# Kernel tuning notes

Measured on AMD Instinct MI355X. Metric: run time of the kernel, lower is better.

## Reference

```python
import jax, jax.numpy as jnp
import numpy as np

B, NSM, NLG = 64, 400, 196
SM, LG = 512, 1024
D, H, DH = 4, 16, 64
INNER = H * DH
EPS = 1e-5


def setup_inputs() -> dict:
    key = jax.random.key(0)
    ks = iter(jax.random.split(key, 40))
    def rn(shape, s=0.02):
        return jax.random.normal(next(ks), shape, jnp.float32) * s
    inp = {
        "sm_tokens": rn((B, NSM + 1, SM), 1.0),
        "lg_tokens": rn((B, NLG + 1, LG), 1.0),
    }
    def branch(p, din, dout):
        inp[p + "_pin_w"] = rn((D, din, dout))
        inp[p + "_pin_b"] = jnp.zeros((D, dout), jnp.float32)
        inp[p + "_ng"] = jnp.ones((D, dout), jnp.float32)
        inp[p + "_nb"] = jnp.zeros((D, dout), jnp.float32)
        inp[p + "_wq"] = rn((D, dout, INNER))
        inp[p + "_wkv"] = rn((D, dout, 2 * INNER))
        inp[p + "_wo"] = rn((D, INNER, dout))
        inp[p + "_wob"] = jnp.zeros((D, dout), jnp.float32)
        inp[p + "_pout_w"] = rn((D, dout, din))
        inp[p + "_pout_b"] = jnp.zeros((D, din), jnp.float32)
    branch("a", SM, LG)   # sm_attend_lg: project sm->lg, attention in lg_dim
    branch("b", LG, SM)   # lg_attend_sm: project lg->sm, attention in sm_dim
    return inp


def _attn(cls_tok, ctx, ng, nb, wq, wkv, wo, wob):
    # cls_tok: [B,1,dim]; ctx: [B,S,dim]. Matches lucidrains cross_vit Attention:
    # LayerNorm(x) first; kv context = concat(normed_x, context); context NOT normed.
    scale = DH ** -0.5
    mu = cls_tok.mean(-1, keepdims=True)
    var = ((cls_tok - mu) ** 2).mean(-1, keepdims=True)
    xn = (cls_tok - mu) * jax.lax.rsqrt(var + EPS) * ng + nb
    c = jnp.concatenate([xn, ctx], axis=1)             # kv_include_self=True
    q = (xn @ wq).reshape(B, 1, H, DH)
    k, v = jnp.split(c @ wkv, 2, axis=-1)
    k = k.reshape(B, -1, H, DH)
    v = v.reshape(B, -1, H, DH)
    s = jnp.einsum('bqhd,bkhd->bhqk', q, k) * scale     # [B,H,1,S+1]
    p = jax.nn.softmax(s, axis=-1)
    o = jnp.einsum('bhqk,bkhd->bqhd', p, v).reshape(B, 1, INNER)
    return o @ wo + wob


def _forward(sm_tokens, lg_tokens,
             a_pin_w, a_pin_b, a_ng, a_nb, a_wq, a_wkv, a_wo, a_wob, a_pout_w, a_pout_b,
             b_pin_w, b_pin_b, b_ng, b_nb, b_wq, b_wkv, b_wo, b_wob, b_pout_w, b_pout_b):
    sm_cls, sm_patch = sm_tokens[:, :1], sm_tokens[:, 1:]
    lg_cls, lg_patch = lg_tokens[:, :1], lg_tokens[:, 1:]
    for i in range(D):
        x = sm_cls @ a_pin_w[i] + a_pin_b[i]
        x = _attn(x, lg_patch, a_ng[i], a_nb[i], a_wq[i], a_wkv[i], a_wo[i], a_wob[i])
        sm_cls = x @ a_pout_w[i] + a_pout_b[i] + sm_cls
        y = lg_cls @ b_pin_w[i] + b_pin_b[i]
        y = _attn(y, sm_patch, b_ng[i], b_nb[i], b_wq[i], b_wkv[i], b_wo[i], b_wob[i])
        lg_cls = y @ b_pout_w[i] + b_pout_b[i] + lg_cls
    sm_out = jnp.concatenate([sm_cls, sm_patch], axis=1)
    lg_out = jnp.concatenate([lg_cls, lg_patch], axis=1)
    return sm_out, lg_out


def reference(sm_tokens, lg_tokens,
              a_pin_w, a_pin_b, a_ng, a_nb, a_wq, a_wkv, a_wo, a_wob, a_pout_w, a_pout_b,
              b_pin_w, b_pin_b, b_ng, b_nb, b_wq, b_wkv, b_wo, b_wob, b_pout_w, b_pout_b):
    return _forward(sm_tokens, lg_tokens,
                    a_pin_w, a_pin_b, a_ng, a_nb, a_wq, a_wkv, a_wo, a_wob, a_pout_w, a_pout_b,
                    b_pin_w, b_pin_b, b_ng, b_nb, b_wq, b_wkv, b_wo, b_wob, b_pout_w, b_pout_b)
```

## Files before the change

kernel.cpp:

```cpp
#include <hip/hip_runtime.h>
#include <hip/hip_bf16.h>
#include <math.h>

#define B_     64
#define NSM_   400
#define NLG_   196
#define SM_    512
#define LG_    1024
#define H_     16
#define DH_    64
#define INNER_ 1024
#define SSTR   424
#define PSTR   424

typedef __attribute__((ext_vector_type(8))) short bf16x8;
typedef __attribute__((ext_vector_type(8))) unsigned short u16x8;
typedef __attribute__((ext_vector_type(4))) float f32x4;

__device__ __forceinline__ unsigned short f2b(float f) {
  unsigned u = __float_as_uint(f);
  u = u + 0x7FFFu + ((u >> 16) & 1u);
  return (unsigned short)(u >> 16);
}
__device__ __forceinline__ f32x4 zero4() {
  f32x4 a; a[0] = 0.f; a[1] = 0.f; a[2] = 0.f; a[3] = 0.f; return a;
}


struct CC2 { const float* tok; float* out; unsigned short* abf; float* cls;
             unsigned short* clsb; int Np1, nf4, shift, tot4; };
struct WTDesc { const float* src; unsigned short* dst; unsigned short* dst2; int K, N; };
struct WTArgs { WTDesc d[10]; int cum[11]; };
__global__ __launch_bounds__(256) void setup1(CC2 ca, CC2 cb, WTArgs W, int nw) {
  __shared__ unsigned short tile[64][68];
  const int tid = threadIdx.x;
  if ((int)blockIdx.x < nw) {
    int bx = blockIdx.x, di = 0;
    while (bx >= W.cum[di + 1]) di++;
    int local = bx - W.cum[di];
    WTDesc g = W.d[di];
    int tn = g.N >> 6;
    int tpl = tn * (g.K >> 6);
    int layer = local / tpl, rem = local % tpl;
    int kt = (rem / tn) * 64, nt = (rem % tn) * 64;
    const float* wp = g.src + (size_t)layer * g.K * g.N;
    unsigned short* op = g.dst + (size_t)layer * g.K * g.N;
    unsigned short* d2 = (g.dst2 && nt < 1024)
                             ? g.dst2 + (size_t)layer * g.K * 1024 : nullptr;
#pragma unroll
    for (int p = 0; p < 4; p++) {
      int r = (tid >> 4) + p * 16;
      int c = (tid & 15) * 4;
      const f32x4 v = __builtin_nontemporal_load(
          (const f32x4*)&wp[(size_t)(kt + r) * g.N + nt + c]);
      ushort4 w4;
      w4.x = f2b(v.x); w4.y = f2b(v.y); w4.z = f2b(v.z); w4.w = f2b(v.w);
      *(ushort4*)&tile[r][c] = w4;
      if (d2) *(ushort4*)&d2[(size_t)(kt + r) * 1024 + nt + c] = w4;
    }
    __syncthreads();
    const int r2 = tid >> 2, cseg = tid & 3;
    u16x8 v0, v1;
#pragma unroll
    for (int i = 0; i < 8; i++) v0[i] = tile[cseg * 16 + i][r2];
#pragma unroll
    for (int i = 0; i < 8; i++) v1[i] = tile[cseg * 16 + 8 + i][r2];
    unsigned short* orow = &op[(size_t)(nt + r2) * g.K + kt + cseg * 16];
    *(u16x8*)&orow[0] = v0;
    *(u16x8*)&orow[8] = v1;
  } else {
    const int nblk = gridDim.x - nw;
    const int total = ca.tot4 + cb.tot4;
    for (int i = ((int)blockIdx.x - nw) * 256 + tid; i < total; i += nblk * 256) {
      CC2 g; int idx;
      if (i < ca.tot4) { g = ca; idx = i; } else { g = cb; idx = i - ca.tot4; }
      int rowg = idx >> g.shift, t = idx & ((1 << g.shift) - 1);
      int bb = rowg / g.Np1, row = rowg - bb * g.Np1;
      const f32x4 v = __builtin_nontemporal_load(&((const f32x4*)g.tok)[idx]);
      __builtin_nontemporal_store(v, &((f32x4*)g.out)[idx]);
      ushort4 w2; w2.x = f2b(v.x); w2.y = f2b(v.y); w2.z = f2b(v.z); w2.w = f2b(v.w);
      if (row > 0) {
        ((ushort4*)g.abf)[(size_t)(bb * (g.Np1 - 1) + row - 1) * g.nf4 + t] = w2;
      } else {
        ((f32x4*)g.cls)[(size_t)bb * g.nf4 + t] = v;
        ((ushort4*)g.clsb)[(size_t)bb * g.nf4 + t] = w2;
      }
    }
  }
}

struct TXArgs { const unsigned short* xbf; unsigned short* xT; int Nctx, dout, xstride, nx, ny, nblk; };
__global__ __launch_bounds__(256) void setup2(TXArgs ta, TXArgs tb) {
  __shared__ unsigned short tile[64][68];
  TXArgs g; int bx = blockIdx.x;
  if (bx < ta.nblk) { g = ta; } else { g = tb; bx -= ta.nblk; }
  int cx = bx % g.nx; int rem = bx / g.nx;
  int jy = rem % g.ny; int b = rem / g.ny;
  int jt = jy * 64, ct = cx * 64;
  const int tid = threadIdx.x;
#pragma unroll
  for (int p = 0; p < 4; p++) {
    int row = (tid >> 4) + p * 16;
    int c = (tid & 15) * 4;
    int j = jt + row;
    ushort4 v;
    if (j < g.Nctx) v = *(const ushort4*)&g.xbf[((size_t)b * g.Nctx + j) * g.dout + ct + c];
    else { v.x = 0; v.y = 0; v.z = 0; v.w = 0; }
    *(ushort4*)&tile[row][c] = v;
  }
  __syncthreads();
  const int r2 = tid >> 2, jseg = tid & 3;
  if (jt + jseg * 16 < g.xstride) {
    u16x8 v0, v1;
#pragma unroll
    for (int i = 0; i < 8; i++) v0[i] = tile[jseg * 16 + i][r2];
#pragma unroll
    for (int i = 0; i < 8; i++) v1[i] = tile[jseg * 16 + 8 + i][r2];
    unsigned short* orow = &g.xT[((size_t)b * g.dout + ct + r2) * g.xstride + jt + jseg * 16];
    *(u16x8*)&orow[0] = v0;
    *(u16x8*)&orow[8] = v1;
  }
}

struct SGDesc {
  const unsigned short* A; const unsigned short* WT; const float* bias;
  float* Cf; unsigned short* Cbf; const float* Rf;
  int K, N;
  float* outF; int ostride;
};
struct SGArgs { SGDesc d[4]; int cum[5]; int nd; };
__global__ __launch_bounds__(256) void sg_wide(SGArgs W) {
  int bx = blockIdx.x, di = 0;
  while (di < W.nd - 1 && bx >= W.cum[di + 1]) di++;
  SGDesc g = W.d[di];
  const int n0 = (bx - W.cum[di]) * 16;
  const int tid = threadIdx.x;
  const int lane = tid & 63, mt = tid >> 6;
  const int r16 = lane & 15, kv8 = (lane >> 4) * 8;
  f32x4 acc0 = zero4(), acc1 = zero4();
  const unsigned short* wp = &g.WT[(size_t)(n0 + r16) * g.K + kv8];
  const unsigned short* ap = &g.A[(size_t)(mt * 16 + r16) * g.K + kv8];
  const int K = g.K;
#pragma unroll 2
  for (int k0 = 0; k0 < K; k0 += 64) {
    acc0 = __builtin_amdgcn_mfma_f32_16x16x32_bf16(*(const bf16x8*)&ap[k0],
                                                   *(const bf16x8*)&wp[k0], acc0, 0, 0, 0);
    acc1 = __builtin_amdgcn_mfma_f32_16x16x32_bf16(*(const bf16x8*)&ap[k0 + 32],
                                                   *(const bf16x8*)&wp[k0 + 32], acc1, 0, 0, 0);
  }
  const int rbase = (lane >> 4) * 4;
#pragma unroll
  for (int rr = 0; rr < 4; rr++) {
    int r = mt * 16 + rbase + rr, c = n0 + r16;
    float v = acc0[rr] + acc1[rr];
    if (g.bias) v += g.bias[c];
    if (g.Rf) v += g.Rf[(size_t)r * g.N + c];
    if (g.Cf)  g.Cf[(size_t)r * g.N + c] = v;
    if (g.Cbf) g.Cbf[(size_t)r * g.N + c] = f2b(v);
    if (g.outF) g.outF[(size_t)r * g.ostride + c] = v;
  }
}

struct LNArgs { const float* x; unsigned short* xnb; const float* ng; const float* nb; int dim; };
__global__ __launch_bounds__(256) void ln2(LNArgs la, LNArgs lb) {
  LNArgs g = ((int)blockIdx.x < 64) ? la : lb;
  int b = blockIdx.x & 63, t = threadIdx.x;
  __shared__ float rs[4], rq[4], bc[2];
  const float* xp = g.x + (size_t)b * g.dim;
  float s = 0.f, sq = 0.f;
  for (int c = t; c < g.dim; c += 256) {
    float v = xp[c];
    s += v; sq += v * v;
  }
#pragma unroll
  for (int off = 32; off >= 1; off >>= 1) {
    s += __shfl_down(s, off);
    sq += __shfl_down(sq, off);
  }
  int w = t >> 6;
  if ((t & 63) == 0) { rs[w] = s; rq[w] = sq; }
  __syncthreads();
  if (t == 0) {
    float ts = rs[0] + rs[1] + rs[2] + rs[3];
    float tq = rq[0] + rq[1] + rq[2] + rq[3];
    float mu = ts / g.dim;
    float var = tq / g.dim - mu * mu;
    bc[0] = mu; bc[1] = rsqrtf(var + 1e-5f);
  }
  __syncthreads();
  float mu = bc[0], r = bc[1];
  for (int c = t; c < g.dim; c += 256)
    g.xnb[(size_t)b * g.dim + c] = f2b((xp[c] - mu) * r * g.ng[c] + g.nb[c]);
}

struct QTArgs { const unsigned short* qb16; const unsigned short* wkvnb;
                unsigned short* qt; int dout, ntiles, nblk; };
__global__ __launch_bounds__(256) void qtilde3(QTArgs ga, QTArgs gb) {
  QTArgs g; int bx = blockIdx.x;
  if (bx < ga.nblk) g = ga; else { g = gb; bx -= ga.nblk; }
  const int h = bx / g.ntiles, nt = bx - h * g.ntiles;
  const int n0 = nt * 16;
  const int tid = threadIdx.x, lane = tid & 63, mt = tid >> 6;
  const int r16 = lane & 15, kv8 = (lane >> 4) * 8;
  const unsigned short* ap = g.qb16 + (size_t)(mt * 16 + r16) * INNER_ + h * 64 + kv8;
  const unsigned short* bp = g.wkvnb + (size_t)(n0 + r16) * 1024 + h * 64 + kv8;
  f32x4 acc0 = zero4(), acc1 = zero4();
  acc0 = __builtin_amdgcn_mfma_f32_16x16x32_bf16(*(const bf16x8*)&ap[0],
                                                 *(const bf16x8*)&bp[0], acc0, 0, 0, 0);
  acc1 = __builtin_amdgcn_mfma_f32_16x16x32_bf16(*(const bf16x8*)&ap[32],
                                                 *(const bf16x8*)&bp[32], acc1, 0, 0, 0);
  const int rbase = (lane >> 4) * 4;
#pragma unroll
  for (int rr = 0; rr < 4; rr++) {
    int b = mt * 16 + rbase + rr;
    g.qt[((size_t)b * 16 + h) * g.dout + n0 + r16] = f2b(acc0[rr] + acc1[rr]);
  }
}

struct SArgs { const unsigned short* qt; const unsigned short* xbf; float* S;
               int dout, Nctx, ntj, nbj, nblk; };
__global__ __launch_bounds__(256) void s_gemm(SArgs ga, SArgs gb) {
  SArgs g; int bx;
  if ((int)blockIdx.x < ga.nblk) { g = ga; bx = blockIdx.x; }
  else { g = gb; bx = blockIdx.x - ga.nblk; }
  const int per8 = g.nblk >> 3;
  const int logical = (bx & 7) * per8 + (bx >> 3);
  const int b = logical / g.nbj, jq = logical - b * g.nbj;
  const int tid = threadIdx.x, lane = tid & 63, w = tid >> 6;
  const int jt = jq * 4 + w;
  if (jt >= g.ntj) return;
  const int r16 = lane & 15, kv8 = (lane >> 4) * 8;
  const unsigned short* ap = g.qt + ((size_t)b * 16 + r16) * g.dout + kv8;
  const unsigned short* bp = g.xbf + ((size_t)b * g.Nctx + jt * 16 + r16) * g.dout + kv8;
  f32x4 acc0 = zero4(), acc1 = zero4();
  const int K = g.dout;
#pragma unroll 2
  for (int k0 = 0; k0 < K; k0 += 64) {
    acc0 = __builtin_amdgcn_mfma_f32_16x16x32_bf16(*(const bf16x8*)&ap[k0],
                                                   *(const bf16x8*)&bp[k0], acc0, 0, 0, 0);
    acc1 = __builtin_amdgcn_mfma_f32_16x16x32_bf16(*(const bf16x8*)&ap[k0 + 32],
                                                   *(const bf16x8*)&bp[k0 + 32], acc1, 0, 0, 0);
  }
  const int rbase = (lane >> 4) * 4;
#pragma unroll
  for (int rr = 0; rr < 4; rr++)
    g.S[((size_t)b * 16 + rbase + rr) * SSTR + jt * 16 + r16] = acc0[rr] + acc1[rr];
}

struct SMArgs { const float* S; const float* qb; const float* kvc;
                unsigned short* p; float* pcls; int Nctx, Npad; };
__global__ __launch_bounds__(256) void softmax_p2(SMArgs ga, SMArgs gb) {
  SMArgs g = blockIdx.z ? gb : ga;
  const int h = blockIdx.x, b = blockIdx.y;
  const int t = threadIdx.x;
  __shared__ float red[4], bc;
  float sc = 0.f;
  if (t < 64) sc = g.qb[(size_t)b * INNER_ + h * 64 + t] * g.kvc[(size_t)b * 2048 + h * 64 + t];
#pragma unroll
  for (int o = 32; o >= 1; o >>= 1) sc += __shfl_down(sc, o);
  if (t == 0) bc = sc * 0.125f;
  __syncthreads();
  const float scls = bc;
  const float* Sp = g.S + ((size_t)b * 16 + h) * SSTR;

  float sraw[2] = {-1e30f, -1e30f};
#pragma unroll
  for (int u2 = 0; u2 < 2; u2++) {
    int j = t + u2 * 256;
    if (j < g.Nctx) sraw[u2] = Sp[j] * 0.125f;
  }
  float mx = fmaxf(fmaxf(sraw[0], sraw[1]), scls);
#pragma unroll
  for (int o = 32; o >= 1; o >>= 1) mx = fmaxf(mx, __shfl_down(mx, o));
  if ((t & 63) == 0) red[t >> 6] = mx;
  __syncthreads();
  mx = fmaxf(fmaxf(red[0], red[1]), fmaxf(red[2], red[3]));
  __syncthreads();

  float e0 = (t < g.Nctx) ? expf(sraw[0] - mx) : 0.f;
  float e1 = (t + 256 < g.Nctx) ? expf(sraw[1] - mx) : 0.f;
  float ecls = expf(scls - mx);
  float ls = e0 + e1;
#pragma unroll
  for (int o = 32; o >= 1; o >>= 1) ls += __shfl_down(ls, o);
  if ((t & 63) == 0) red[t >> 6] = ls;
  __syncthreads();
  const float denom = red[0] + red[1] + red[2] + red[3] + ecls;
  const float inv = 1.f / denom;

  unsigned short* pp = g.p + ((size_t)b * 16 + h) * PSTR;
  if (t < g.Nctx) pp[t] = f2b(e0 * inv);
  if (t + 256 < g.Nctx) pp[t + 256] = f2b(e1 * inv);
  for (int j = g.Nctx + t; j < g.Npad; j += 256) pp[j] = 0;
  if (t == 0) g.pcls[b * 16 + h] = ecls * inv;
}

struct UG { const unsigned short* p; const unsigned short* xT; unsigned short* u;
            int dout, Npad, xstride, ntx; };
__global__ __launch_bounds__(256) void ugemm2(UG ga, UG gb) {
  const int bid = blockIdx.x;
  const int logical = (bid & 7) * 192 + (bid >> 3);
  const int b = logical / 24;
  int x = logical - b * 24;
  UG g;
  if (x < ga.ntx) g = ga; else { g = gb; x -= ga.ntx; }
  const int tid = threadIdx.x, lane = tid & 63, w = tid >> 6;
  const int c0 = x * 64 + w * 16;
  const int r16 = lane & 15, kv8 = (lane >> 4) * 8, rbase = (lane >> 4) * 4;
  const unsigned short* ap = g.p + ((size_t)b * 16 + r16) * PSTR + kv8;
  const unsigned short* bp = g.xT + ((size_t)b * g.dout + c0 + r16) * g.xstride + kv8;
  f32x4 acc0 = zero4(), acc1 = zero4();
  const int Kp = g.Npad;
  int k0 = 0;
  for (; k0 + 64 <= Kp; k0 += 64) {
    acc0 = __builtin_amdgcn_mfma_f32_16x16x32_bf16(*(const bf16x8*)&ap[k0],
                                                   *(const bf16x8*)&bp[k0], acc0, 0, 0, 0);
    acc1 = __builtin_amdgcn_mfma_f32_16x16x32_bf16(*(const bf16x8*)&ap[k0 + 32],
                                                   *(const bf16x8*)&bp[k0 + 32], acc1, 0, 0, 0);
  }
  if (k0 < Kp)
    acc0 = __builtin_amdgcn_mfma_f32_16x16x32_bf16(*(const bf16x8*)&ap[k0],
                                                   *(const bf16x8*)&bp[k0], acc0, 0, 0, 0);
#pragma unroll
  for (int rr = 0; rr < 4; rr++)
    g.u[((size_t)b * 16 + rbase + rr) * g.dout + c0 + r16] = f2b(acc0[rr] + acc1[rr]);
}

struct OArgs {
  const unsigned short* u; const unsigned short* WTkv; const float* kvc; const float* pcls;
  unsigned short* ob; int dout;
};
__global__ __launch_bounds__(256) void ogemm_w(OArgs ga, OArgs gb) {
  OArgs g; int bx = blockIdx.x;
  if (bx < 64) { g = ga; } else { g = gb; bx -= 64; }
  const int h = bx >> 2, dt = bx & 3;
  const int tid = threadIdx.x, lane = tid & 63, mt = tid >> 6;
  const int r16 = lane & 15, kv8 = (lane >> 4) * 8;
  const int dout = g.dout;
  f32x4 acc0 = zero4(), acc1 = zero4();
  const unsigned short* wp = &g.WTkv[(size_t)(1024 + h * 64 + dt * 16 + r16) * dout + kv8];
  const unsigned short* up = &g.u[((size_t)(mt * 16 + r16) * 16 + h) * dout + kv8];
#pragma unroll 2
  for (int k0 = 0; k0 < dout; k0 += 64) {
    acc0 = __builtin_amdgcn_mfma_f32_16x16x32_bf16(*(const bf16x8*)&up[k0],
                                                   *(const bf16x8*)&wp[k0], acc0, 0, 0, 0);
    acc1 = __builtin_amdgcn_mfma_f32_16x16x32_bf16(*(const bf16x8*)&up[k0 + 32],
                                                   *(const bf16x8*)&wp[k0 + 32], acc1, 0, 0, 0);
  }
  const int rbase = (lane >> 4) * 4;
#pragma unroll
  for (int rr = 0; rr < 4; rr++) {
    int bi = mt * 16 + rbase + rr;
    int d = h * 64 + dt * 16 + r16;
    float v = acc0[rr] + acc1[rr] + g.pcls[bi * 16 + h] * g.kvc[(size_t)bi * 2048 + 1024 + d];
    g.ob[(size_t)bi * INNER_ + d] = f2b(v);
  }
}

extern "C" void kernel_launch(void* const* d_in, const int* in_sizes, int n_in,
                              void* d_out, int out_size, void* d_ws, size_t ws_size,
                              hipStream_t stream) {
  const float* sm_tokens = (const float*)d_in[0];
  const float* lg_tokens = (const float*)d_in[1];
  const float* a_pin_w  = (const float*)d_in[2];  const float* a_pin_b  = (const float*)d_in[3];
  const float* a_ng     = (const float*)d_in[4];  const float* a_nb     = (const float*)d_in[5];
  const float* a_wq     = (const float*)d_in[6];  const float* a_wkv    = (const float*)d_in[7];
  const float* a_wo     = (const float*)d_in[8];  const float* a_wob    = (const float*)d_in[9];
  const float* a_pout_w = (const float*)d_in[10]; const float* a_pout_b = (const float*)d_in[11];
  const float* b_pin_w  = (const float*)d_in[12]; const float* b_pin_b  = (const float*)d_in[13];
  const float* b_ng     = (const float*)d_in[14]; const float* b_nb     = (const float*)d_in[15];
  const float* b_wq     = (const float*)d_in[16]; const float* b_wkv    = (const float*)d_in[17];
  const float* b_wo     = (const float*)d_in[18]; const float* b_wob    = (const float*)d_in[19];
  const float* b_pout_w = (const float*)d_in[20]; const float* b_pout_b = (const float*)d_in[21];

  float* out = (float*)d_out;
  char* ws = (char*)d_ws;
  size_t off = 0;
  auto alloc = [&](size_t bytes) -> void* {
    void* pt = ws + off;
    off += (bytes + 255) & ~(size_t)255;
    return pt;
  };
  unsigned short* Abf_lg = (unsigned short*)alloc(((size_t)B_ * NLG_ + 32) * LG_ * 2);
  unsigned short* Abf_sm = (unsigned short*)alloc(((size_t)B_ * NSM_ + 32) * SM_ * 2);
  unsigned short* xT_lg  = (unsigned short*)alloc((size_t)B_ * LG_ * 224 * 2);
  unsigned short* xT_sm  = (unsigned short*)alloc((size_t)B_ * SM_ * 416 * 2);
  unsigned short* WTkv_a = (unsigned short*)alloc((size_t)4 * 2048 * LG_ * 2);
  unsigned short* WTkv_b = (unsigned short*)alloc((size_t)4 * 2048 * SM_ * 2);
  unsigned short* wkvnb_a = (unsigned short*)alloc((size_t)4 * LG_ * 1024 * 2);
  unsigned short* wkvnb_b = (unsigned short*)alloc((size_t)4 * SM_ * 1024 * 2);
  unsigned short* WTpin_a = (unsigned short*)alloc((size_t)4 * SM_ * LG_ * 2);
  unsigned short* WTpin_b = (unsigned short*)alloc((size_t)4 * LG_ * SM_ * 2);
  unsigned short* WTwq_a  = (unsigned short*)alloc((size_t)4 * LG_ * INNER_ * 2);
  unsigned short* WTwq_b  = (unsigned short*)alloc((size_t)4 * SM_ * INNER_ * 2);
  unsigned short* WTwo_a  = (unsigned short*)alloc((size_t)4 * INNER_ * LG_ * 2);
  unsigned short* WTwo_b  = (unsigned short*)alloc((size_t)4 * INNER_ * SM_ * 2);
  unsigned short* WTpout_a = (unsigned short*)alloc((size_t)4 * LG_ * SM_ * 2);
  unsigned short* WTpout_b = (unsigned short*)alloc((size_t)4 * SM_ * LG_ * 2);
  unsigned short* qt_a = (unsigned short*)alloc((size_t)B_ * 16 * LG_ * 2);
  unsigned short* qt_b = (unsigned short*)alloc((size_t)B_ * 16 * SM_ * 2);
  float* S_a = (float*)alloc((size_t)B_ * 16 * SSTR * 4);
  float* S_b = (float*)alloc((size_t)B_ * 16 * SSTR * 4);
  unsigned short* p_a = (unsigned short*)alloc((size_t)B_ * 16 * PSTR * 2);
  unsigned short* p_b = (unsigned short*)alloc((size_t)B_ * 16 * PSTR * 2);
  unsigned short* u_a  = (unsigned short*)alloc((size_t)B_ * 16 * LG_ * 2);
  unsigned short* u_b  = (unsigned short*)alloc((size_t)B_ * 16 * SM_ * 2);
  float* pcls_a = (float*)alloc((size_t)B_ * 16 * 4);
  float* pcls_b = (float*)alloc((size_t)B_ * 16 * 4);
  float* cls_sm = (float*)alloc((size_t)B_ * SM_ * 4);
  float* cls_lg = (float*)alloc((size_t)B_ * LG_ * 4);
  unsigned short* clsb_sm = (unsigned short*)alloc((size_t)B_ * SM_ * 2);
  unsigned short* clsb_lg = (unsigned short*)alloc((size_t)B_ * LG_ * 2);
  float* xbuf_a = (float*)alloc((size_t)B_ * LG_ * 4);
  float* xbuf_b = (float*)alloc((size_t)B_ * SM_ * 4);
  unsigned short* xnb_a = (unsigned short*)alloc((size_t)B_ * LG_ * 2);
  unsigned short* xnb_b = (unsigned short*)alloc((size_t)B_ * SM_ * 2);
  float* qbuf_a = (float*)alloc((size_t)B_ * INNER_ * 4);
  float* qbuf_b = (float*)alloc((size_t)B_ * INNER_ * 4);
  unsigned short* qb16_a = (unsigned short*)alloc((size_t)B_ * INNER_ * 2);
  unsigned short* qb16_b = (unsigned short*)alloc((size_t)B_ * INNER_ * 2);
  float* kvc_a  = (float*)alloc((size_t)B_ * 2048 * 4);
  float* kvc_b  = (float*)alloc((size_t)B_ * 2048 * 4);
  unsigned short* obufb_a = (unsigned short*)alloc((size_t)B_ * INNER_ * 2);
  unsigned short* obufb_b = (unsigned short*)alloc((size_t)B_ * INNER_ * 2);
  unsigned short* t1b_a = (unsigned short*)alloc((size_t)B_ * LG_ * 2);
  unsigned short* t1b_b = (unsigned short*)alloc((size_t)B_ * SM_ * 2);
  (void)ws_size; (void)in_sizes; (void)n_in; (void)out_size;

  const size_t sm_elems = (size_t)B_ * (NSM_ + 1) * SM_;

  CC2 ca{sm_tokens, out, Abf_sm, cls_sm, clsb_sm, NSM_ + 1, SM_ / 4, 7,
         (int)(sm_elems / 4)};
  CC2 cb{lg_tokens, out + sm_elems, Abf_lg, cls_lg, clsb_lg, NLG_ + 1, LG_ / 4, 8,
         (int)((size_t)B_ * (NLG_ + 1) * LG_ / 4)};
  WTArgs W;
  W.d[0] = {a_wkv,    WTkv_a,   wkvnb_a, LG_, 2048};
  W.d[1] = {b_wkv,    WTkv_b,   wkvnb_b, SM_, 2048};
  W.d[2] = {a_pin_w,  WTpin_a,  nullptr, SM_, LG_};
  W.d[3] = {b_pin_w,  WTpin_b,  nullptr, LG_, SM_};
  W.d[4] = {a_wq,     WTwq_a,   nullptr, LG_, INNER_};
  W.d[5] = {b_wq,     WTwq_b,   nullptr, SM_, INNER_};
  W.d[6] = {a_wo,     WTwo_a,   nullptr, INNER_, LG_};
  W.d[7] = {b_wo,     WTwo_b,   nullptr, INNER_, SM_};
  W.d[8] = {a_pout_w, WTpout_a, nullptr, LG_, SM_};
  W.d[9] = {b_pout_w, WTpout_b, nullptr, SM_, LG_};
  W.cum[0] = 0;
  for (int i = 0; i < 10; i++)
    W.cum[i + 1] = W.cum[i] + (W.d[i].K / 64) * (W.d[i].N / 64) * 4;
  setup1<<<W.cum[10] + 2048, 256, 0, stream>>>(ca, cb, W, W.cum[10]);
  TXArgs txa{Abf_lg, xT_lg, NLG_, LG_, 224, LG_ / 64, 4, B_ * (LG_ / 64) * 4};
  TXArgs txb{Abf_sm, xT_sm, NSM_, SM_, 416, SM_ / 64, 7, B_ * (SM_ / 64) * 7};
  setup2<<<txa.nblk + txb.nblk, 256, 0, stream>>>(txa, txb);

  for (int l = 0; l < 4; l++) {
    const unsigned short* WTpin_al = WTpin_a + (size_t)l * SM_ * LG_;
    const unsigned short* WTpin_bl = WTpin_b + (size_t)l * LG_ * SM_;
    const unsigned short* WTwq_al  = WTwq_a  + (size_t)l * LG_ * INNER_;
    const unsigned short* WTwq_bl  = WTwq_b  + (size_t)l * SM_ * INNER_;
    const unsigned short* WTkv_al  = WTkv_a  + (size_t)l * 2048 * LG_;
    const unsigned short* WTkv_bl  = WTkv_b  + (size_t)l * 2048 * SM_;
    const unsigned short* wkvnb_al = wkvnb_a + (size_t)l * LG_ * 1024;
    const unsigned short* wkvnb_bl = wkvnb_b + (size_t)l * SM_ * 1024;
    const unsigned short* WTwo_al  = WTwo_a  + (size_t)l * INNER_ * LG_;
    const unsigned short* WTwo_bl  = WTwo_b  + (size_t)l * INNER_ * SM_;
    const unsigned short* WTpout_al = WTpout_a + (size_t)l * LG_ * SM_;
    const unsigned short* WTpout_bl = WTpout_b + (size_t)l * SM_ * LG_;

    SGArgs Gp; Gp.nd = 2;
    Gp.d[0] = {clsb_sm, WTpin_al, a_pin_b + (size_t)l * LG_, xbuf_a, nullptr, nullptr, SM_, LG_, nullptr, 0};
    Gp.d[1] = {clsb_lg, WTpin_bl, b_pin_b + (size_t)l * SM_, xbuf_b, nullptr, nullptr, LG_, SM_, nullptr, 0};
    Gp.cum[0] = 0; Gp.cum[1] = LG_ / 16; Gp.cum[2] = LG_ / 16 + SM_ / 16;
    sg_wide<<<Gp.cum[2], 256, 0, stream>>>(Gp);
    LNArgs la{xbuf_a, xnb_a, a_ng + (size_t)l * LG_, a_nb + (size_t)l * LG_, LG_};
    LNArgs lb{xbuf_b, xnb_b, b_ng + (size_t)l * SM_, b_nb + (size_t)l * SM_, SM_};
    ln2<<<128, 256, 0, stream>>>(la, lb);
    SGArgs Gq; Gq.nd = 4;
    Gq.d[0] = {xnb_a, WTwq_al, nullptr, qbuf_a, qb16_a, nullptr, LG_, INNER_, nullptr, 0};
    Gq.d[1] = {xnb_a, WTkv_al, nullptr, kvc_a,  nullptr, nullptr, LG_, 2048, nullptr, 0};
    Gq.d[2] = {xnb_b, WTwq_bl, nullptr, qbuf_b, qb16_b, nullptr, SM_, INNER_, nullptr, 0};
    Gq.d[3] = {xnb_b, WTkv_bl, nullptr, kvc_b,  nullptr, nullptr, SM_, 2048, nullptr, 0};
    Gq.cum[0] = 0; Gq.cum[1] = 64; Gq.cum[2] = 192; Gq.cum[3] = 256; Gq.cum[4] = 384;
    sg_wide<<<384, 256, 0, stream>>>(Gq);
    QTArgs qa{qb16_a, wkvnb_al, qt_a, LG_, LG_ / 16, 16 * (LG_ / 16)};
    QTArgs qb{qb16_b, wkvnb_bl, qt_b, SM_, SM_ / 16, 16 * (SM_ / 16)};
    qtilde3<<<qa.nblk + qb.nblk, 256, 0, stream>>>(qa, qb);
    SArgs sa{qt_a, Abf_lg, S_a, LG_, NLG_, 14, 4, B_ * 4};
    SArgs sb{qt_b, Abf_sm, S_b, SM_, NSM_, 26, 7, B_ * 7};
    s_gemm<<<sa.nblk + sb.nblk, 256, 0, stream>>>(sa, sb);
    SMArgs ma{S_a, qbuf_a, kvc_a, p_a, pcls_a, NLG_, 224};
    SMArgs mb{S_b, qbuf_b, kvc_b, p_b, pcls_b, NSM_, 416};
    softmax_p2<<<dim3(H_, B_, 2), 256, 0, stream>>>(ma, mb);
    UG ua{p_a, xT_lg, u_a, LG_, 224, 224, LG_ / 64};
    UG ub{p_b, xT_sm, u_b, SM_, 416, 416, SM_ / 64};
    ugemm2<<<1536, 256, 0, stream>>>(ua, ub);
    OArgs oa{u_a, WTkv_al, kvc_a, pcls_a, obufb_a, LG_};
    OArgs ob{u_b, WTkv_bl, kvc_b, pcls_b, obufb_b, SM_};
    ogemm_w<<<128, 256, 0, stream>>>(oa, ob);
    SGArgs Gw; Gw.nd = 2;
    Gw.d[0] = {obufb_a, WTwo_al, a_wob + (size_t)l * LG_, nullptr, t1b_a, nullptr, INNER_, LG_, nullptr, 0};
    Gw.d[1] = {obufb_b, WTwo_bl, b_wob + (size_t)l * SM_, nullptr, t1b_b, nullptr, INNER_, SM_, nullptr, 0};
    Gw.cum[0] = 0; Gw.cum[1] = LG_ / 16; Gw.cum[2] = LG_ / 16 + SM_ / 16;
    sg_wide<<<Gw.cum[2], 256, 0, stream>>>(Gw);
    float* outF_a = (l == 3) ? out : nullptr;
    float* outF_b = (l == 3) ? out + sm_elems : nullptr;
    SGArgs Gr; Gr.nd = 2;
    Gr.d[0] = {t1b_a, WTpout_al, a_pout_b + (size_t)l * SM_, cls_sm, clsb_sm, cls_sm, LG_, SM_,
               outF_a, (NSM_ + 1) * SM_};
    Gr.d[1] = {t1b_b, WTpout_bl, b_pout_b + (size_t)l * LG_, cls_lg, clsb_lg, cls_lg, SM_, LG_,
               outF_b, (NLG_ + 1) * LG_};
    Gr.cum[0] = 0; Gr.cum[1] = SM_ / 16; Gr.cum[2] = SM_ / 16 + LG_ / 16;
    sg_wide<<<Gr.cum[2], 256, 0, stream>>>(Gr);
  }
}
```

Measured before the change: 488.0 us.

## Fold self-token into context attention path, drop per-layer K/V projection of CLS

Treats the normalized CLS token as an extra context row: layernorm writes it into the transposed context buffer and s_gemm reads it (or a zero row) as key column Nctx. The softmax no longer computes a separate CLS score, and ogemm drops the pcls*v correction, so the per-layer 2048-wide KV projection of the CLS token is removed from the query GEMM launch. Weight preparation is restructured to emit only the V half transposed and the K half straight. This trades a larger GEMM launch and a scalar side path for a few scattered writes and extra branching in s_gemm.

```diff
diff --git a/kernel.cpp b/kernel.cpp
--- a/kernel.cpp
+++ b/kernel.cpp
@@ -29,45 +29,63 @@
 
 struct CC2 { const float* tok; float* out; unsigned short* abf; float* cls;
              unsigned short* clsb; int Np1, nf4, shift, tot4; };
-struct WTDesc { const float* src; unsigned short* dst; unsigned short* dst2; int K, N; };
-struct WTArgs { WTDesc d[10]; int cum[11]; };
-__global__ __launch_bounds__(256) void setup1(CC2 ca, CC2 cb, WTArgs W, int nw) {
+struct WTDesc { const float* src; unsigned short* dstT; unsigned short* dstS;
+                int K, Ntiles, srcStride, colOff; };
+struct WTArgs { WTDesc d[12]; int cum[13]; };
+__global__ __launch_bounds__(256) void setup1(CC2 ca, CC2 cb, WTArgs W, int nw,
+                                              unsigned short* zb) {
   __shared__ unsigned short tile[64][68];
   const int tid = threadIdx.x;
+  if (blockIdx.x == 0) {
+    ushort4 z; z.x = 0; z.y = 0; z.z = 0; z.w = 0;
+    ((ushort4*)zb)[tid] = z;
+  }
   if ((int)blockIdx.x < nw) {
     int bx = blockIdx.x, di = 0;
     while (bx >= W.cum[di + 1]) di++;
     int local = bx - W.cum[di];
     WTDesc g = W.d[di];
-    int tn = g.N >> 6;
+    int tn = g.Ntiles;
     int tpl = tn * (g.K >> 6);
     int layer = local / tpl, rem = local % tpl;
     int kt = (rem / tn) * 64, nt = (rem % tn) * 64;
-    const float* wp = g.src + (size_t)layer * g.K * g.N;
-    unsigned short* op = g.dst + (size_t)layer * g.K * g.N;
-    unsigned short* d2 = (g.dst2 && nt < 1024)
-                             ? g.dst2 + (size_t)layer * g.K * 1024 : nullptr;
-#pragma unroll
-    for (int p = 0; p < 4; p++) {
-      int r = (tid >> 4) + p * 16;
-      int c = (tid & 15) * 4;
-      const f32x4 v = __builtin_nontemporal_load(
-          (const f32x4*)&wp[(size_t)(kt + r) * g.N + nt + c]);
-      ushort4 w4;
-      w4.x = f2b(v.x); w4.y = f2b(v.y); w4.z = f2b(v.z); w4.w = f2b(v.w);
-      *(ushort4*)&tile[r][c] = w4;
-      if (d2) *(ushort4*)&d2[(size_t)(kt + r) * 1024 + nt + c] = w4;
+    const float* wp = g.src + (size_t)layer * g.K * g.srcStride;
+    unsigned short* dS = g.dstS ? g.dstS + (size_t)layer * g.K * 1024 : nullptr;
+    if (!g.dstT) {
+#pragma unroll
+      for (int p = 0; p < 4; p++) {
+        int r = (tid >> 4) + p * 16;
+        int c = (tid & 15) * 4;
+        const f32x4 v = __builtin_nontemporal_load(
+            (const f32x4*)&wp[(size_t)(kt + r) * g.srcStride + g.colOff + nt + c]);
+        ushort4 w4;
+        w4.x = f2b(v.x); w4.y = f2b(v.y); w4.z = f2b(v.z); w4.w = f2b(v.w);
+        *(ushort4*)&dS[(size_t)(kt + r) * 1024 + nt + c] = w4;
+      }
+    } else {
+      unsigned short* op = g.dstT + (size_t)layer * (g.Ntiles * 64) * g.K;
+#pragma unroll
+      for (int p = 0; p < 4; p++) {
+        int r = (tid >> 4) + p * 16;
+        int c = (tid & 15) * 4;
+        const f32x4 v = __builtin_nontemporal_load(
+            (const f32x4*)&wp[(size_t)(kt + r) * g.srcStride + g.colOff + nt + c]);
+        ushort4 w4;
+        w4.x = f2b(v.x); w4.y = f2b(v.y); w4.z = f2b(v.z); w4.w = f2b(v.w);
+        *(ushort4*)&tile[r][c] = w4;
+        if (dS) *(ushort4*)&dS[(size_t)(kt + r) * 1024 + nt + c] = w4;
+      }
+      __syncthreads();
+      const int r2 = tid >> 2, cseg = tid & 3;
+      u16x8 v0, v1;
+#pragma unroll
+      for (int i = 0; i < 8; i++) v0[i] = tile[cseg * 16 + i][r2];
+#pragma unroll
+      for (int i = 0; i < 8; i++) v1[i] = tile[cseg * 16 + 8 + i][r2];
+      unsigned short* orow = &op[(size_t)(nt + r2) * g.K + kt + cseg * 16];
+      *(u16x8*)&orow[0] = v0;
+      *(u16x8*)&orow[8] = v1;
     }
-    __syncthreads();
-    const int r2 = tid >> 2, cseg = tid & 3;
-    u16x8 v0, v1;
-#pragma unroll
-    for (int i = 0; i < 8; i++) v0[i] = tile[cseg * 16 + i][r2];
-#pragma unroll
-    for (int i = 0; i < 8; i++) v1[i] = tile[cseg * 16 + 8 + i][r2];
-    unsigned short* orow = &op[(size_t)(nt + r2) * g.K + kt + cseg * 16];
-    *(u16x8*)&orow[0] = v0;
-    *(u16x8*)&orow[8] = v1;
   } else {
     const int nblk = gridDim.x - nw;
     const int total = ca.tot4 + cb.tot4;
@@ -161,7 +179,8 @@
   }
 }
 
-struct LNArgs { const float* x; unsigned short* xnb; const float* ng; const float* nb; int dim; };
+struct LNArgs { const float* x; unsigned short* xnb; const float* ng; const float* nb;
+                int dim; unsigned short* xT; int xstr, jcls; };
 __global__ __launch_bounds__(256) void ln2(LNArgs la, LNArgs lb) {
   LNArgs g = ((int)blockIdx.x < 64) ? la : lb;
   int b = blockIdx.x & 63, t = threadIdx.x;
@@ -189,8 +208,11 @@
   }
   __syncthreads();
   float mu = bc[0], r = bc[1];
-  for (int c = t; c < g.dim; c += 256)
-    g.xnb[(size_t)b * g.dim + c] = f2b((xp[c] - mu) * r * g.ng[c] + g.nb[c]);
+  for (int c = t; c < g.dim; c += 256) {
+    unsigned short hv = f2b((xp[c] - mu) * r * g.ng[c] + g.nb[c]);
+    g.xnb[(size_t)b * g.dim + c] = hv;
+    g.xT[((size_t)b * g.dim + c) * g.xstr + g.jcls] = hv;
+  }
 }
 
 struct QTArgs { const unsigned short* qb16; const unsigned short* wkvnb;
@@ -217,7 +239,8 @@
   }
 }
 
-struct SArgs { const unsigned short* qt; const unsigned short* xbf; float* S;
+struct SArgs { const unsigned short* qt; const unsigned short* xbf;
+               const unsigned short* xnb; const unsigned short* zb; float* S;
                int dout, Nctx, ntj, nbj, nblk; };
 __global__ __launch_bounds__(256) void s_gemm(SArgs ga, SArgs gb) {
   SArgs g; int bx;
@@ -230,8 +253,13 @@
   const int jt = jq * 4 + w;
   if (jt >= g.ntj) return;
   const int r16 = lane & 15, kv8 = (lane >> 4) * 8;
+  const int j = jt * 16 + r16;
+  const unsigned short* brow;
+  if (j < g.Nctx)       brow = g.xbf + ((size_t)b * g.Nctx + j) * g.dout;
+  else if (j == g.Nctx) brow = g.xnb + (size_t)b * g.dout;
+  else                  brow = g.zb;
   const unsigned short* ap = g.qt + ((size_t)b * 16 + r16) * g.dout + kv8;
-  const unsigned short* bp = g.xbf + ((size_t)b * g.Nctx + jt * 16 + r16) * g.dout + kv8;
+  const unsigned short* bp = brow + kv8;
   f32x4 acc0 = zero4(), acc1 = zero4();
   const int K = g.dout;
 #pragma unroll 2
@@ -247,29 +275,21 @@
     g.S[((size_t)b * 16 + rbase + rr) * SSTR + jt * 16 + r16] = acc0[rr] + acc1[rr];
 }
 
-struct SMArgs { const float* S; const float* qb; const float* kvc;
-                unsigned short* p; float* pcls; int Nctx, Npad; };
+struct SMArgs { const float* S; unsigned short* p; int Nk, Npad; };
 __global__ __launch_bounds__(256) void softmax_p2(SMArgs ga, SMArgs gb) {
   SMArgs g = blockIdx.z ? gb : ga;
   const int h = blockIdx.x, b = blockIdx.y;
   const int t = threadIdx.x;
-  __shared__ float red[4], bc;
-  float sc = 0.f;
-  if (t < 64) sc = g.qb[(size_t)b * INNER_ + h * 64 + t] * g.kvc[(size_t)b * 2048 + h * 64 + t];
-#pragma unroll
-  for (int o = 32; o >= 1; o >>= 1) sc += __shfl_down(sc, o);
-  if (t == 0) bc = sc * 0.125f;
-  __syncthreads();
-  const float scls = bc;
+  __shared__ float red[4];
   const float* Sp = g.S + ((size_t)b * 16 + h) * SSTR;
 
   float sraw[2] = {-1e30f, -1e30f};
 #pragma unroll
   for (int u2 = 0; u2 < 2; u2++) {
     int j = t + u2 * 256;
-    if (j < g.Nctx) sraw[u2] = Sp[j] * 0.125f;
-  }
-  float mx = fmaxf(fmaxf(sraw[0], sraw[1]), scls);
+    if (j < g.Nk) sraw[u2] = Sp[j] * 0.125f;
+  }
+  float mx = fmaxf(sraw[0], sraw[1]);
 #pragma unroll
   for (int o = 32; o >= 1; o >>= 1) mx = fmaxf(mx, __shfl_down(mx, o));
   if ((t & 63) == 0) red[t >> 6] = mx;
@@ -277,22 +297,20 @@
   mx = fmaxf(fmaxf(red[0], red[1]), fmaxf(red[2], red[3]));
   __syncthreads();
 
-  float e0 = (t < g.Nctx) ? expf(sraw[0] - mx) : 0.f;
-  float e1 = (t + 256 < g.Nctx) ? expf(sraw[1] - mx) : 0.f;
-  float ecls = expf(scls - mx);
+  float e0 = (t < g.Nk) ? expf(sraw[0] - mx) : 0.f;
+  float e1 = (t + 256 < g.Nk) ? expf(sraw[1] - mx) : 0.f;
   float ls = e0 + e1;
 #pragma unroll
   for (int o = 32; o >= 1; o >>= 1) ls += __shfl_down(ls, o);
   if ((t & 63) == 0) red[t >> 6] = ls;
   __syncthreads();
-  const float denom = red[0] + red[1] + red[2] + red[3] + ecls;
+  const float denom = red[0] + red[1] + red[2] + red[3];
   const float inv = 1.f / denom;
 
   unsigned short* pp = g.p + ((size_t)b * 16 + h) * PSTR;
-  if (t < g.Nctx) pp[t] = f2b(e0 * inv);
-  if (t + 256 < g.Nctx) pp[t + 256] = f2b(e1 * inv);
-  for (int j = g.Nctx + t; j < g.Npad; j += 256) pp[j] = 0;
-  if (t == 0) g.pcls[b * 16 + h] = ecls * inv;
+  if (t < g.Nk) pp[t] = f2b(e0 * inv);
+  if (t + 256 < g.Nk) pp[t + 256] = f2b(e1 * inv);
+  for (int j = g.Nk + t; j < g.Npad; j += 256) pp[j] = 0;
 }
 
 struct UG { const unsigned short* p; const unsigned short* xT; unsigned short* u;
@@ -327,8 +345,7 @@
 }
 
 struct OArgs {
-  const unsigned short* u; const unsigned short* WTkv; const float* kvc; const float* pcls;
-  unsigned short* ob; int dout;
+  const unsigned short* u; const unsigned short* WTv; unsigned short* ob; int dout;
 };
 __global__ __launch_bounds__(256) void ogemm_w(OArgs ga, OArgs gb) {
   OArgs g; int bx = blockIdx.x;
@@ -338,7 +355,7 @@
   const int r16 = lane & 15, kv8 = (lane >> 4) * 8;
   const int dout = g.dout;
   f32x4 acc0 = zero4(), acc1 = zero4();
-  const unsigned short* wp = &g.WTkv[(size_t)(1024 + h * 64 + dt * 16 + r16) * dout + kv8];
+  const unsigned short* wp = &g.WTv[(size_t)(h * 64 + dt * 16 + r16) * dout + kv8];
   const unsigned short* up = &g.u[((size_t)(mt * 16 + r16) * 16 + h) * dout + kv8];
 #pragma unroll 2
   for (int k0 = 0; k0 < dout; k0 += 64) {
@@ -352,8 +369,7 @@
   for (int rr = 0; rr < 4; rr++) {
     int bi = mt * 16 + rbase + rr;
     int d = h * 64 + dt * 16 + r16;
-    float v = acc0[rr] + acc1[rr] + g.pcls[bi * 16 + h] * g.kvc[(size_t)bi * 2048 + 1024 + d];
-    g.ob[(size_t)bi * INNER_ + d] = f2b(v);
+    g.ob[(size_t)bi * INNER_ + d] = f2b(acc0[rr] + acc1[rr]);
   }
 }
 
@@ -385,8 +401,8 @@
   unsigned short* Abf_sm = (unsigned short*)alloc(((size_t)B_ * NSM_ + 32) * SM_ * 2);
   unsigned short* xT_lg  = (unsigned short*)alloc((size_t)B_ * LG_ * 224 * 2);
   unsigned short* xT_sm  = (unsigned short*)alloc((size_t)B_ * SM_ * 416 * 2);
-  unsigned short* WTkv_a = (unsigned short*)alloc((size_t)4 * 2048 * LG_ * 2);
-  unsigned short* WTkv_b = (unsigned short*)alloc((size_t)4 * 2048 * SM_ * 2);
+  unsigned short* WTv_a  = (unsigned short*)alloc((size_t)4 * 1024 * LG_ * 2);
+  unsigned short* WTv_b  = (unsigned short*)alloc((size_t)4 * 1024 * SM_ * 2);
   unsigned short* wkvnb_a = (unsigned short*)alloc((size_t)4 * LG_ * 1024 * 2);
   unsigned short* wkvnb_b = (unsigned short*)alloc((size_t)4 * SM_ * 1024 * 2);
   unsigned short* WTpin_a = (unsigned short*)alloc((size_t)4 * SM_ * LG_ * 2);
@@ -405,8 +421,6 @@
   unsigned short* p_b = (unsigned short*)alloc((size_t)B_ * 16 * PSTR * 2);
   unsigned short* u_a  = (unsigned short*)alloc((size_t)B_ * 16 * LG_ * 2);
   unsigned short* u_b  = (unsigned short*)alloc((size_t)B_ * 16 * SM_ * 2);
-  float* pcls_a = (float*)alloc((size_t)B_ * 16 * 4);
-  float* pcls_b = (float*)alloc((size_t)B_ * 16 * 4);
   float* cls_sm = (float*)alloc((size_t)B_ * SM_ * 4);
   float* cls_lg = (float*)alloc((size_t)B_ * LG_ * 4);
   unsigned short* clsb_sm = (unsigned short*)alloc((size_t)B_ * SM_ * 2);
@@ -419,12 +433,11 @@
   float* qbuf_b = (float*)alloc((size_t)B_ * INNER_ * 4);
   unsigned short* qb16_a = (unsigned short*)alloc((size_t)B_ * INNER_ * 2);
   unsigned short* qb16_b = (unsigned short*)alloc((size_t)B_ * INNER_ * 2);
-  float* kvc_a  = (float*)alloc((size_t)B_ * 2048 * 4);
-  float* kvc_b  = (float*)alloc((size_t)B_ * 2048 * 4);
   unsigned short* obufb_a = (unsigned short*)alloc((size_t)B_ * INNER_ * 2);
   unsigned short* obufb_b = (unsigned short*)alloc((size_t)B_ * INNER_ * 2);
   unsigned short* t1b_a = (unsigned short*)alloc((size_t)B_ * LG_ * 2);
   unsigned short* t1b_b = (unsigned short*)alloc((size_t)B_ * SM_ * 2);
+  unsigned short* zb = (unsigned short*)alloc(1024 * 2);
   (void)ws_size; (void)in_sizes; (void)n_in; (void)out_size;
 
   const size_t sm_elems = (size_t)B_ * (NSM_ + 1) * SM_;
@@ -434,20 +447,22 @@
   CC2 cb{lg_tokens, out + sm_elems, Abf_lg, cls_lg, clsb_lg, NLG_ + 1, LG_ / 4, 8,
          (int)((size_t)B_ * (NLG_ + 1) * LG_ / 4)};
   WTArgs W;
-  W.d[0] = {a_wkv,    WTkv_a,   wkvnb_a, LG_, 2048};
-  W.d[1] = {b_wkv,    WTkv_b,   wkvnb_b, SM_, 2048};
-  W.d[2] = {a_pin_w,  WTpin_a,  nullptr, SM_, LG_};
-  W.d[3] = {b_pin_w,  WTpin_b,  nullptr, LG_, SM_};
-  W.d[4] = {a_wq,     WTwq_a,   nullptr, LG_, INNER_};
-  W.d[5] = {b_wq,     WTwq_b,   nullptr, SM_, INNER_};
-  W.d[6] = {a_wo,     WTwo_a,   nullptr, INNER_, LG_};
-  W.d[7] = {b_wo,     WTwo_b,   nullptr, INNER_, SM_};
-  W.d[8] = {a_pout_w, WTpout_a, nullptr, LG_, SM_};
-  W.d[9] = {b_pout_w, WTpout_b, nullptr, SM_, LG_};
+  W.d[0]  = {a_wkv,    nullptr,  wkvnb_a, LG_,   16, 2048, 0};
+  W.d[1]  = {a_wkv,    WTv_a,    nullptr, LG_,   16, 2048, 1024};
+  W.d[2]  = {b_wkv,    nullptr,  wkvnb_b, SM_,   16, 2048, 0};
+  W.d[3]  = {b_wkv,    WTv_b,    nullptr, SM_,   16, 2048, 1024};
+  W.d[4]  = {a_pin_w,  WTpin_a,  nullptr, SM_,   16, 1024, 0};
+  W.d[5]  = {b_pin_w,  WTpin_b,  nullptr, LG_,    8,  512, 0};
+  W.d[6]  = {a_wq,     WTwq_a,   nullptr, LG_,   16, 1024, 0};
+  W.d[7]  = {b_wq,     WTwq_b,   nullptr, SM_,   16, 1024, 0};
+  W.d[8]  = {a_wo,     WTwo_a,   nullptr, INNER_,16, 1024, 0};
+  W.d[9]  = {b_wo,     WTwo_b,   nullptr, INNER_, 8,  512, 0};
+  W.d[10] = {a_pout_w, WTpout_a, nullptr, LG_,    8,  512, 0};
+  W.d[11] = {b_pout_w, WTpout_b, nullptr, SM_,   16, 1024, 0};
   W.cum[0] = 0;
-  for (int i = 0; i < 10; i++)
-    W.cum[i + 1] = W.cum[i] + (W.d[i].K / 64) * (W.d[i].N / 64) * 4;
-  setup1<<<W.cum[10] + 2048, 256, 0, stream>>>(ca, cb, W, W.cum[10]);
+  for (int i = 0; i < 12; i++)
+    W.cum[i + 1] = W.cum[i] + (W.d[i].K / 64) * W.d[i].Ntiles * 4;
+  setup1<<<W.cum[12] + 2048, 256, 0, stream>>>(ca, cb, W, W.cum[12], zb);
   TXArgs txa{Abf_lg, xT_lg, NLG_, LG_, 224, LG_ / 64, 4, B_ * (LG_ / 64) * 4};
   TXArgs txb{Abf_sm, xT_sm, NSM_, SM_, 416, SM_ / 64, 7, B_ * (SM_ / 64) * 7};
   setup2<<<txa.nblk + txb.nblk, 256, 0, stream>>>(txa, txb);
@@ -457,8 +472,8 @@
     const unsigned short* WTpin_bl = WTpin_b + (size_t)l * LG_ * SM_;
     const unsigned short* WTwq_al  = WTwq_a  + (size_t)l * LG_ * INNER_;
     const unsigned short* WTwq_bl  = WTwq_b  + (size_t)l * SM_ * INNER_;
-    const unsigned short* WTkv_al  = WTkv_a  + (size_t)l * 2048 * LG_;
-    const unsigned short* WTkv_bl  = WTkv_b  + (size_t)l * 2048 * SM_;
+    const unsigned short* WTv_al   = WTv_a   + (size_t)l * 1024 * LG_;
+    const unsigned short* WTv_bl   = WTv_b   + (size_t)l * 1024 * SM_;
     const unsigned short* wkvnb_al = wkvnb_a + (size_t)l * LG_ * 1024;
     const unsigned short* wkvnb_bl = wkvnb_b + (size_t)l * SM_ * 1024;
     const unsigned short* WTwo_al  = WTwo_a  + (size_t)l * INNER_ * LG_;
@@ -471,30 +486,28 @@
     Gp.d[1] = {clsb_lg, WTpin_bl, b_pin_b + (size_t)l * SM_, xbuf_b, nullptr, nullptr, LG_, SM_, nullptr, 0};
     Gp.cum[0] = 0; Gp.cum[1] = LG_ / 16; Gp.cum[2] = LG_ / 16 + SM_ / 16;
     sg_wide<<<Gp.cum[2], 256, 0, stream>>>(Gp);
-    LNArgs la{xbuf_a, xnb_a, a_ng + (size_t)l * LG_, a_nb + (size_t)l * LG_, LG_};
-    LNArgs lb{xbuf_b, xnb_b, b_ng + (size_t)l * SM_, b_nb + (size_t)l * SM_, SM_};
+    LNArgs la{xbuf_a, xnb_a, a_ng + (size_t)l * LG_, a_nb + (size_t)l * LG_, LG_, xT_lg, 224, NLG_};
+    LNArgs lb{xbuf_b, xnb_b, b_ng + (size_t)l * SM_, b_nb + (size_t)l * SM_, SM_, xT_sm, 416, NSM_};
     ln2<<<128, 256, 0, stream>>>(la, lb);
-    SGArgs Gq; Gq.nd = 4;
+    SGArgs Gq; Gq.nd = 2;
     Gq.d[0] = {xnb_a, WTwq_al, nullptr, qbuf_a, qb16_a, nullptr, LG_, INNER_, nullptr, 0};
-    Gq.d[1] = {xnb_a, WTkv_al, nullptr, kvc_a,  nullptr, nullptr, LG_, 2048, nullptr, 0};
-    Gq.d[2] = {xnb_b, WTwq_bl, nullptr, qbuf_b, qb16_b, nullptr, SM_, INNER_, nullptr, 0};
-    Gq.d[3] = {xnb_b, WTkv_bl, nullptr, kvc_b,  nullptr, nullptr, SM_, 2048, nullptr, 0};
-    Gq.cum[0] = 0; Gq.cum[1] = 64; Gq.cum[2] = 192; Gq.cum[3] = 256; Gq.cum[4] = 384;
-    sg_wide<<<384, 256, 0, stream>>>(Gq);
+    Gq.d[1] = {xnb_b, WTwq_bl, nullptr, qbuf_b, qb16_b, nullptr, SM_, INNER_, nullptr, 0};
+    Gq.cum[0] = 0; Gq.cum[1] = 64; Gq.cum[2] = 128;
+    sg_wide<<<128, 256, 0, stream>>>(Gq);
     QTArgs qa{qb16_a, wkvnb_al, qt_a, LG_, LG_ / 16, 16 * (LG_ / 16)};
     QTArgs qb{qb16_b, wkvnb_bl, qt_b, SM_, SM_ / 16, 16 * (SM_ / 16)};
     qtilde3<<<qa.nblk + qb.nblk, 256, 0, stream>>>(qa, qb);
-    SArgs sa{qt_a, Abf_lg, S_a, LG_, NLG_, 14, 4, B_ * 4};
-    SArgs sb{qt_b, Abf_sm, S_b, SM_, NSM_, 26, 7, B_ * 7};
+    SArgs sa{qt_a, Abf_lg, xnb_a, zb, S_a, LG_, NLG_, 14, 4, B_ * 4};
+    SArgs sb{qt_b, Abf_sm, xnb_b, zb, S_b, SM_, NSM_, 26, 7, B_ * 7};
     s_gemm<<<sa.nblk + sb.nblk, 256, 0, stream>>>(sa, sb);
-    SMArgs ma{S_a, qbuf_a, kvc_a, p_a, pcls_a, NLG_, 224};
-    SMArgs mb{S_b, qbuf_b, kvc_b, p_b, pcls_b, NSM_, 416};
+    SMArgs ma{S_a, p_a, NLG_ + 1, 224};
+    SMArgs mb{S_b, p_b, NSM_ + 1, 416};
     softmax_p2<<<dim3(H_, B_, 2), 256, 0, stream>>>(ma, mb);
     UG ua{p_a, xT_lg, u_a, LG_, 224, 224, LG_ / 64};
     UG ub{p_b, xT_sm, u_b, SM_, 416, 416, SM_ / 64};
     ugemm2<<<1536, 256, 0, stream>>>(ua, ub);
-    OArgs oa{u_a, WTkv_al, kvc_a, pcls_a, obufb_a, LG_};
-    OArgs ob{u_b, WTkv_bl, kvc_b, pcls_b, obufb_b, SM_};
+    OArgs oa{u_a, WTv_al, obufb_a, LG_};
+    OArgs ob{u_b, WTv_bl, obufb_b, SM_};
     ogemm_w<<<128, 256, 0, stream>>>(oa, ob);
     SGArgs Gw; Gw.nd = 2;
     Gw.d[0] = {obufb_a, WTwo_al, a_wob + (size_t)l * LG_, nullptr, t1b_a, nullptr, INNER_, LG_, nullptr, 0};
```

Result: faster. 473.3 us (median of 2 runs) (-3.0%).
